# Optimization experiments

Hardware: AMD Instinct MI355X
Metric: run time of the kernel (lower is better)

## Reference

```python
import jax, jax.numpy as jnp
import numpy as np

C = 5.0          # tanh clamp constant (args.c, non-trainable)
B, N, R, D = 4, 16, 64, 256  # batch, block_num, block_len, word_dim
NEG = -1e9


def setup_inputs() -> dict:
    key = jax.random.key(0)
    ks = iter(jax.random.split(key, 80))

    def W(i, o):
        # xavier-like init (torch stores (out,in); we store (in,out) and use x @ W)
        return jax.random.normal(next(ks), (i, o), jnp.float32) * np.float32(np.sqrt(2.0 / (i + o)))

    def bvec(d):
        return jax.random.normal(next(ks), (d,), jnp.float32) * 0.01

    inp = {"x": jax.random.normal(next(ks), (B, N, R, D), jnp.float32)}
    for p in ("fw", "bw"):
        inp[f"fcW_{p}"] = W(D, D);  inp[f"fcb_{p}"] = bvec(D)
        inp[f"mW1_{p}"] = W(D, D);  inp[f"mW2_{p}"] = W(D, D);  inp[f"mb_{p}"] = bvec(D)
        inp[f"s2tW1_{p}"] = W(D, D); inp[f"s2tb1_{p}"] = bvec(D)
        inp[f"s2tW_{p}"] = W(D, D);  inp[f"s2tb_{p}"] = bvec(D)
        inp[f"gW1_{p}"] = W(D, D);  inp[f"gW2_{p}"] = W(D, D);  inp[f"gb_{p}"] = bvec(D)
        inp[f"fW1_{p}"] = W(3 * D, D); inp[f"fb1_{p}"] = bvec(D)
        inp[f"fW2_{p}"] = W(3 * D, D); inp[f"fb2_{p}"] = bvec(D)
    return inp


def _mSA(x, W1, W2, b, fw):
    # x: (..., L, d) -> (..., L, d). Additive per-feature attention with strict
    # triangular mask. fw: token i attends to j > i (last row zeroed);
    # bw: token i attends to j < i (first row zeroed). Matches the torch
    # -inf mask + narrow + zero-pad construction exactly.
    L = x.shape[-2]
    xi = (x @ W1)[..., :, None, :]                 # (..., L, 1, d)
    xj = (x @ W2)[..., None, :, :]                 # (..., 1, L, d)
    f = C * jnp.tanh((xi + xj + b) / C)            # (..., i, j, d)
    i = jnp.arange(L)[:, None]
    j = jnp.arange(L)[None, :]
    allowed = (j > i) if fw else (j < i)           # (L, L)
    scores = jnp.where(allowed[..., None], f, NEG)
    att = jax.nn.softmax(scores, axis=-2)          # softmax over j
    rowvalid = (jnp.arange(L) < L - 1) if fw else (jnp.arange(L) > 0)
    att = att * rowvalid[:, None, None].astype(x.dtype)
    return jnp.einsum('...ijd,...jd->...id', att, x)


def _s2t(x, W1, b1, Wo, bo):
    # source2token self-attention: (..., L, d) -> (..., d)
    f = jax.nn.relu(x @ W1 + b1)
    a = jax.nn.softmax(f @ Wo + bo, axis=-2)
    return jnp.sum(a * x, axis=-2)


def _mblosa(x, mW1, mW2, mb, s2tW1, s2tb1, s2tW, s2tb,
            gW1, gW2, gb, fW1, fb1, fW2, fb2, fw):
    Bb, n, r, d = x.shape
    h = _mSA(x, mW1, mW2, mb, fw)                  # (B, n, r, d) intra-block
    v = _s2t(h, s2tW1, s2tb1, s2tW, s2tb)          # (B, n, d)    block summary
    o = _mSA(v, mW1, mW2, mb, fw)                  # (B, n, d)    inter-block
    G = jax.nn.sigmoid(o @ gW1 + v @ gW2 + gb)
    e = G * o + (1.0 - G) * v                      # (B, n, d)
    # torch: cat of e[i] repeated r times, then narrow(1, 0, n)
    idx = jnp.arange(n) // r
    E = e[:, idx]                                  # (B, n, d)
    # torch: flatten blocks then narrow(1, 0, n) (faithful to source)
    xf = x.reshape(Bb, n * r, d)[:, :n]
    hf = h.reshape(Bb, n * r, d)[:, :n]
    cat = jnp.concatenate([xf, hf, E], axis=-1)    # (B, n, 3d)
    fusion = jax.nn.relu(cat @ fW1 + fb1)
    Gf = jax.nn.sigmoid(cat @ fW2 + fb2)
    return Gf * fusion + (1.0 - Gf) * xf           # (B, n, d)


def reference(x,
              fcW_fw, fcb_fw, mW1_fw, mW2_fw, mb_fw, s2tW1_fw, s2tb1_fw,
              s2tW_fw, s2tb_fw, gW1_fw, gW2_fw, gb_fw, fW1_fw, fb1_fw,
              fW2_fw, fb2_fw,
              fcW_bw, fcb_bw, mW1_bw, mW2_bw, mb_bw, s2tW1_bw, s2tb1_bw,
              s2tW_bw, s2tb_bw, gW1_bw, gW2_bw, gb_bw, fW1_bw, fb1_bw,
              fW2_bw, fb2_bw):
    in_fw = jax.nn.relu(x @ fcW_fw + fcb_fw)
    in_bw = jax.nn.relu(x @ fcW_bw + fcb_bw)
    u_fw = _mblosa(in_fw, mW1_fw, mW2_fw, mb_fw, s2tW1_fw, s2tb1_fw,
                   s2tW_fw, s2tb_fw, gW1_fw, gW2_fw, gb_fw,
                   fW1_fw, fb1_fw, fW2_fw, fb2_fw, True)
    u_bw = _mblosa(in_bw, mW1_bw, mW2_bw, mb_bw, s2tW1_bw, s2tb1_bw,
                   s2tW_bw, s2tb_bw, gW1_bw, gW2_bw, gb_bw,
                   fW1_bw, fb1_bw, fW2_bw, fb2_bw, False)
    return jnp.concatenate([u_fw, u_bw], axis=-1)  # (B, n, 2d)
```

## Files before the change

### kernel.cpp

```cpp
#include <hip/hip_runtime.h>
#include <hip/hip_bf16.h>

typedef __hip_bfloat16 BF16;
typedef __attribute__((ext_vector_type(8))) short short8;
typedef __attribute__((ext_vector_type(4))) float f32x4;

#define MFMA_B16(a,b,c) __builtin_amdgcn_mfma_f32_16x16x32_bf16((a),(b),(c),0,0,0)

#if __has_builtin(__builtin_amdgcn_exp2f)
#define EXP2F(x) __builtin_amdgcn_exp2f(x)
#else
#define EXP2F(x) __expf(0.6931471805599453f * (x))
#endif

__device__ __forceinline__ short f2bs(float f){ BF16 h = __float2bfloat16(f); return *(short*)&h; }
__device__ __forceinline__ float bs2f(short s){ BF16 h = *(BF16*)&s; return __bfloat162float(h); }

struct SrcPack { const float* s[10]; };

__global__ __launch_bounds__(256) void prep_k(SrcPack p, short* __restrict__ Oh,
                                              short* __restrict__ Ol)
{
    __shared__ float s[64][65];
    const float* W = p.s[blockIdx.y];
    short* oh = Oh + (size_t)blockIdx.y * 65536;
    short* ol = Ol + (size_t)blockIdx.y * 65536;
    int tr = (blockIdx.x >> 2) * 64, tc = (blockIdx.x & 3) * 64;
    #pragma unroll
    for (int i = 0; i < 16; i++) {
        int e = threadIdx.x + i * 256;
        int r = e >> 6, c = e & 63;
        s[c][r] = W[(size_t)(tr + r) * 256 + tc + c];
    }
    __syncthreads();
    #pragma unroll
    for (int i = 0; i < 16; i++) {
        int e = threadIdx.x + i * 256;
        int c2 = e >> 6, r2 = e & 63;
        float v = s[c2][r2];
        short hi = f2bs(v);
        short lo = f2bs(v - bs2f(hi));
        size_t oi = (size_t)(tc + c2) * 256 + tr + r2;
        oh[oi] = hi;
        ol[oi] = lo;
    }
}

template<int AM, int OM, int RELU, int BS>
__device__ __forceinline__ void gemm_body(const void* __restrict__ A0,
    const void* __restrict__ Alo,
    const short* __restrict__ Wh, const short* __restrict__ Wl,
    const float* __restrict__ bias, void* __restrict__ O0, void* __restrict__ O1,
    int row0, int col0)
{
    constexpr int LDK = 72;
    __shared__ short sAh[64 * LDK];
    __shared__ short sAl[(AM == 0) ? 8 : 64 * LDK];
    __shared__ short sBh[64 * LDK];
    __shared__ short sBl[BS ? 8 : 64 * LDK];
    int tid = threadIdx.x;
    int w = tid >> 6, l = tid & 63;
    int m = l & 15, q = l >> 4;
    int sr = w * 16 + m;

    f32x4 acc[4];
    #pragma unroll
    for (int cf = 0; cf < 4; cf++) acc[cf] = (f32x4)(0.f);

    for (int kh = 0; kh < 4; kh++) {
        int kbase = kh * 64;
        #pragma unroll
        for (int i = 0; i < 2; i++) {
            int kl = q * 8 + 32 * i;
            size_t gofs = (size_t)(row0 + sr) * 256 + kbase + kl;
            if (AM == 1) {
                const float* src = (const float*)A0 + gofs;
                float4 f0 = *(const float4*)src;
                float4 f1 = *(const float4*)(src + 4);
                short8 vh, vl;
                float tmp[8] = {f0.x, f0.y, f0.z, f0.w, f1.x, f1.y, f1.z, f1.w};
                #pragma unroll
                for (int j = 0; j < 8; j++) {
                    vh[j] = f2bs(tmp[j]);
                    vl[j] = f2bs(tmp[j] - bs2f(vh[j]));
                }
                *(short8*)&sAh[sr * LDK + kl] = vh;
                *(short8*)&sAl[sr * LDK + kl] = vl;
            } else if (AM == 2) {
                *(short8*)&sAh[sr * LDK + kl] = *(const short8*)((const short*)A0 + gofs);
                *(short8*)&sAl[sr * LDK + kl] = *(const short8*)((const short*)Alo + gofs);
            } else {
                *(short8*)&sAh[sr * LDK + kl] = *(const short8*)((const short*)A0 + gofs);
            }
            size_t gofsB = (size_t)(col0 + sr) * 256 + kbase + kl;
            *(short8*)&sBh[sr * LDK + kl] = *(const short8*)(Wh + gofsB);
            if (!BS)
                *(short8*)&sBl[sr * LDK + kl] = *(const short8*)(Wl + gofsB);
        }
        __syncthreads();
        #pragma unroll
        for (int ch = 0; ch < 2; ch++) {
            int k = ch * 32 + q * 8;
            short8 ah = *(const short8*)&sAh[(w * 16 + m) * LDK + k];
            short8 al = (AM != 0) ? *(const short8*)&sAl[(w * 16 + m) * LDK + k] : ah;
            #pragma unroll
            for (int cf = 0; cf < 4; cf++) {
                short8 bh = *(const short8*)&sBh[(cf * 16 + m) * LDK + k];
                acc[cf] = MFMA_B16(ah, bh, acc[cf]);
                if (!BS) {
                    short8 bl = *(const short8*)&sBl[(cf * 16 + m) * LDK + k];
                    acc[cf] = MFMA_B16(ah, bl, acc[cf]);
                }
                if (AM != 0)
                    acc[cf] = MFMA_B16(al, bh, acc[cf]);
            }
        }
        __syncthreads();
    }
    #pragma unroll
    for (int cf = 0; cf < 4; cf++) {
        int col = col0 + cf * 16 + m;
        float bv = bias ? bias[col] : 0.f;
        #pragma unroll
        for (int r = 0; r < 4; r++) {
            int row = row0 + w * 16 + q * 4 + r;
            float v = acc[cf][r] + bv;
            if (RELU) v = fmaxf(v, 0.f);
            size_t oi = (size_t)row * 256 + col;
            if (OM == 0) {
                ((float*)O0)[oi] = v;
            } else if (OM == 1) {
                ((short*)O0)[oi] = f2bs(v);
            } else {
                short hi = f2bs(v);
                ((short*)O0)[oi] = hi;
                ((short*)O1)[oi] = f2bs(v - bs2f(hi));
            }
        }
    }
}

struct GDir { const void* A0; const void* Al; const short* Wh; const short* Wl;
              const float* bias; void* O0; void* O1; };

template<int AM, int OM, int RELU, int BS>
__global__ __launch_bounds__(256) void gemm_k(GDir p0, GDir p1)
{
    GDir p = blockIdx.z ? p1 : p0;
    gemm_body<AM, OM, RELU, BS>(p.A0, p.Al, p.Wh, p.Wl, p.bias, p.O0, p.O1,
                                blockIdx.x * 64, blockIdx.y * 64);
}

struct MbloDir { const short* Ah;
                 const short* W1h; const short* W2h;
                 const float* mb; short* Hh; int fw; };

__global__ __launch_bounds__(512) void mblo_k(MbloDir p0, MbloDir p1)
{
    __shared__ char smraw[33536] __attribute__((aligned(16)));
    short* gAh  = (short*)smraw;
    short* gB1h = gAh + 4608;
    short* gB2h = gAh + 9216;
    float* aP   = (float*)smraw;
    unsigned int* aQX = (unsigned int*)(smraw + 16896);

    const float KLN = -0.06931471805599453f;

    MbloDir p = blockIdx.z ? p1 : p0;
    int tid = threadIdx.x;
    int w = tid >> 6, l = tid & 63;
    int m = l & 15, q = l >> 4;
    int rh = w >> 1;
    int cb = (w & 1) * 2;
    int bn = blockIdx.x >> 1, ipar = blockIdx.x & 1;
    int row0 = bn * 64, d0 = blockIdx.y * 64;
    int srow = tid >> 3;
    int skl  = (tid & 7) * 8;

    f32x4 acc1[2], acc2[2];
    #pragma unroll
    for (int cf = 0; cf < 2; cf++) { acc1[cf] = (f32x4)(0.f); acc2[cf] = (f32x4)(0.f); }

    for (int kh = 0; kh < 4; kh++) {
        int kbase = kh * 64;
        size_t ga = (size_t)(row0 + srow) * 256 + kbase + skl;
        *(short8*)&gAh[srow * 72 + skl] = *(const short8*)(p.Ah + ga);
        size_t gb = (size_t)(d0 + srow) * 256 + kbase + skl;
        *(short8*)&gB1h[srow * 72 + skl] = *(const short8*)(p.W1h + gb);
        *(short8*)&gB2h[srow * 72 + skl] = *(const short8*)(p.W2h + gb);
        __syncthreads();
        #pragma unroll
        for (int ch = 0; ch < 2; ch++) {
            int k = ch * 32 + q * 8;
            short8 ah = *(const short8*)&gAh[(rh * 16 + m) * 72 + k];
            #pragma unroll
            for (int cf = 0; cf < 2; cf++) {
                int bofs = ((cb + cf) * 16 + m) * 72 + k;
                short8 b1 = *(const short8*)&gB1h[bofs];
                acc1[cf] = MFMA_B16(ah, b1, acc1[cf]);
                short8 b2 = *(const short8*)&gB2h[bofs];
                acc2[cf] = MFMA_B16(ah, b2, acc2[cf]);
            }
        }
        __syncthreads();
    }
    short* sQX = (short*)aQX;
    #pragma unroll
    for (int cf = 0; cf < 2; cf++) {
        int col = (cb + cf) * 16 + m;
        float mbv = p.mb[d0 + col];
        #pragma unroll
        for (int r = 0; r < 4; r++) {
            int row = rh * 16 + q * 4 + r;
            aP[row * 66 + col] = __expf(0.4f * acc1[cf][r]) * KLN;
            sQX[col * 130 + 2 * row] = f2bs(__expf(0.4f * (acc2[cf][r] + mbv)));
        }
    }
    {
        size_t gx = (size_t)(row0 + srow) * 256 + d0 + skl;
        short8 xh = *(const short8*)(p.Ah + gx);
        #pragma unroll
        for (int t = 0; t < 8; t++)
            sQX[(skl + t) * 130 + 2 * srow + 1] = xh[t];
    }
    __syncthreads();
    const unsigned int* lane_qx = &aQX[l * 65];
    #pragma unroll
    for (int t8 = 0; t8 < 4; t8++) {
        int i = ipar + 2 * (w + 8 * t8);
        float Pp = aP[i * 66 + l];
        int js = p.fw ? (i + 1) : 0;
        int je = p.fw ? 64 : i;
        float den0 = 0.f, den1 = 0.f, num0 = 0.f, num1 = 0.f;
        int j = js;
        for (; j + 4 <= je; j += 4) {
            unsigned int u0 = lane_qx[j];
            unsigned int u1 = lane_qx[j + 1];
            unsigned int u2 = lane_qx[j + 2];
            unsigned int u3 = lane_qx[j + 3];
            float q0 = bs2f((short)(u0 & 0xffff)), x0 = bs2f((short)(u0 >> 16));
            float q1 = bs2f((short)(u1 & 0xffff)), x1 = bs2f((short)(u1 >> 16));
            float q2 = bs2f((short)(u2 & 0xffff)), x2 = bs2f((short)(u2 >> 16));
            float q3 = bs2f((short)(u3 & 0xffff)), x3 = bs2f((short)(u3 >> 16));
            float w0 = EXP2F(__builtin_amdgcn_rcpf(fmaf(Pp, q0, KLN)));
            float w1 = EXP2F(__builtin_amdgcn_rcpf(fmaf(Pp, q1, KLN)));
            float w2 = EXP2F(__builtin_amdgcn_rcpf(fmaf(Pp, q2, KLN)));
            float w3 = EXP2F(__builtin_amdgcn_rcpf(fmaf(Pp, q3, KLN)));
            den0 += w0; num0 = fmaf(w0, x0, num0);
            den1 += w1; num1 = fmaf(w1, x1, num1);
            den0 += w2; num0 = fmaf(w2, x2, num0);
            den1 += w3; num1 = fmaf(w3, x3, num1);
        }
        for (; j < je; j++) {
            unsigned int u0 = lane_qx[j];
            float q0 = bs2f((short)(u0 & 0xffff)), x0 = bs2f((short)(u0 >> 16));
            float wgt = EXP2F(__builtin_amdgcn_rcpf(fmaf(Pp, q0, KLN)));
            den0 += wgt; num0 = fmaf(wgt, x0, num0);
        }
        float den = den0 + den1, num = num0 + num1;
        bool valid = p.fw ? (i < 63) : (i > 0);
        float out = valid ? (num * __builtin_amdgcn_rcpf(den)) : 0.f;
        p.Hh[(size_t)(row0 + i) * 256 + d0 + l] = f2bs(out);
    }
}

struct S2TDir { const short* Hh; const short* W3h; const float* b1;
                const short* W4h; const float* b2; float* V; };

__global__ __launch_bounds__(512) void s2t_fused_k(S2TDir p0, S2TDir p1)
{
    __shared__ char smraw[79872] __attribute__((aligned(16)));
    short* sT1 = (short*)smraw;
    short* gA  = (short*)(smraw + 33792);
    short* gB  = (short*)(smraw + 43008);
    short* gB2 = (short*)(smraw + 33792);
    float* aL  = (float*)(smraw + 43008);
    float* rm  = (float*)(smraw + 60416);
    float* rd  = rm + 512;
    float* rn  = rm + 1024;

    S2TDir p = blockIdx.z ? p1 : p0;
    int tid = threadIdx.x;
    int w = tid >> 6, l = tid & 63;
    int m = l & 15, q = l >> 4;
    int row0 = blockIdx.x * 64;
    int strip = w >> 1, chalf = w & 1;
    int srow = tid >> 3, skl = (tid & 7) * 8;

    f32x4 acc1[8];
    #pragma unroll
    for (int cf = 0; cf < 8; cf++) acc1[cf] = (f32x4)(0.f);
    for (int kh = 0; kh < 4; kh++) {
        int kbase = kh * 64;
        *(short8*)&gA[srow * 72 + skl] =
            *(const short8*)(p.Hh + (size_t)(row0 + srow) * 256 + kbase + skl);
        int bn = tid >> 1;
        #pragma unroll
        for (int i = 0; i < 4; i++) {
            int kseg = (tid & 1) * 32 + i * 8;
            *(short8*)&gB[bn * 72 + kseg] =
                *(const short8*)(p.W3h + (size_t)bn * 256 + kbase + kseg);
        }
        __syncthreads();
        #pragma unroll
        for (int ch = 0; ch < 2; ch++) {
            int k = ch * 32 + q * 8;
            short8 ah = *(const short8*)&gA[(strip * 16 + m) * 72 + k];
            #pragma unroll
            for (int cf = 0; cf < 8; cf++) {
                short8 bh = *(const short8*)&gB[(chalf * 128 + cf * 16 + m) * 72 + k];
                acc1[cf] = MFMA_B16(ah, bh, acc1[cf]);
            }
        }
        __syncthreads();
    }
    #pragma unroll
    for (int cf = 0; cf < 8; cf++) {
        int col = chalf * 128 + cf * 16 + m;
        float bv = p.b1[col];
        #pragma unroll
        for (int r = 0; r < 4; r++) {
            int row = strip * 16 + q * 4 + r;
            sT1[row * 264 + col] = f2bs(fmaxf(acc1[cf][r] + bv, 0.f));
        }
    }
    __syncthreads();

    for (int dc = 0; dc < 2; dc++) {
        int d0 = (blockIdx.y * 2 + dc) * 64;
        f32x4 acc2[2];
        acc2[0] = (f32x4)(0.f); acc2[1] = (f32x4)(0.f);
        for (int kh = 0; kh < 4; kh++) {
            int kbase = kh * 64;
            *(short8*)&gB2[srow * 72 + skl] =
                *(const short8*)(p.W4h + (size_t)(d0 + srow) * 256 + kbase + skl);
            __syncthreads();
            #pragma unroll
            for (int ch = 0; ch < 2; ch++) {
                int k = ch * 32 + q * 8;
                short8 ah = *(const short8*)&sT1[(strip * 16 + m) * 264 + kbase + k];
                #pragma unroll
                for (int cf = 0; cf < 2; cf++) {
                    short8 bh = *(const short8*)&gB2[(chalf * 32 + cf * 16 + m) * 72 + k];
                    acc2[cf] = MFMA_B16(ah, bh, acc2[cf]);
                }
            }
            __syncthreads();
        }
        #pragma unroll
        for (int cf = 0; cf < 2; cf++) {
            int col = chalf * 32 + cf * 16 + m;
            float bv = p.b2[d0 + col];
            #pragma unroll
            for (int r = 0; r < 4; r++) {
                int row = strip * 16 + q * 4 + r;
                aL[row * 68 + col] = acc2[cf][r] + bv;
            }
        }
        __syncthreads();
        int dl = tid & 63, rq = tid >> 6;
        float mx = -1e30f, den = 0.f, num = 0.f;
        #pragma unroll
        for (int rr = 0; rr < 8; rr++) {
            int r = rq * 8 + rr;
            float lv = aL[r * 68 + dl];
            float hv = bs2f(p.Hh[(size_t)(row0 + r) * 256 + d0 + dl]);
            if (lv > mx) { float sc = __expf(mx - lv); den *= sc; num *= sc; mx = lv; }
            float wgt = __expf(lv - mx);
            den += wgt; num = fmaf(wgt, hv, num);
        }
        rm[rq * 64 + dl] = mx; rd[rq * 64 + dl] = den; rn[rq * 64 + dl] = num;
        __syncthreads();
        if (rq == 0) {
            float M = rm[dl];
            #pragma unroll
            for (int kq = 1; kq < 8; kq++) M = fmaxf(M, rm[kq * 64 + dl]);
            float D = 0.f, Nn = 0.f;
            #pragma unroll
            for (int kq = 0; kq < 8; kq++) {
                float sc = __expf(rm[kq * 64 + dl] - M);
                D += rd[kq * 64 + dl] * sc;
                Nn += rn[kq * 64 + dl] * sc;
            }
            p.V[(size_t)blockIdx.x * 256 + d0 + dl] = Nn / D;
        }
        __syncthreads();
    }
}

struct Gate2Dir { const float* V; const float* W1; const float* W2; const float* mb;
                  const float* gW1; const float* gW2; const float* gb;
                  float* E0; int fw; };

__global__ __launch_bounds__(512) void attn2gate_k(Gate2Dir p0, Gate2Dir p1)
{
    Gate2Dir p = blockIdx.z ? p1 : p0;
    __shared__ __attribute__((aligned(16))) float sVT[4096];
    __shared__ float sPart[16][256];
    __shared__ float so[256], sv[256], red[8][64];
    int tid = threadIdx.x;
    int b = blockIdx.x;
    int k = tid & 255, half = tid >> 8;

    if (p.fw) {
        #pragma unroll
        for (int it = 0; it < 8; it++) {
            int e = tid + it * 512;
            int kk = e >> 4, j = e & 15;
            sVT[e] = p.V[(size_t)(b * 16 + j) * 256 + kk];
        }
        __syncthreads();
        float acc[16];
        #pragma unroll
        for (int j = 0; j < 16; j++) acc[j] = 0.f;
        int kk0 = half * 128;
        #pragma unroll 4
        for (int kk = kk0; kk < kk0 + 128; kk++) {
            const float4* vr = (const float4*)&sVT[kk * 16];
            float4 va = vr[0], vb = vr[1], vc = vr[2], vd = vr[3];
            float w1 = p.W1[(size_t)kk * 256 + k];
            float w2 = p.W2[(size_t)kk * 256 + k];
            acc[0]  = fmaf(va.x, w1, acc[0]);
            acc[1]  = fmaf(va.y, w2, acc[1]);
            acc[2]  = fmaf(va.z, w2, acc[2]);
            acc[3]  = fmaf(va.w, w2, acc[3]);
            acc[4]  = fmaf(vb.x, w2, acc[4]);
            acc[5]  = fmaf(vb.y, w2, acc[5]);
            acc[6]  = fmaf(vb.z, w2, acc[6]);
            acc[7]  = fmaf(vb.w, w2, acc[7]);
            acc[8]  = fmaf(vc.x, w2, acc[8]);
            acc[9]  = fmaf(vc.y, w2, acc[9]);
            acc[10] = fmaf(vc.z, w2, acc[10]);
            acc[11] = fmaf(vc.w, w2, acc[11]);
            acc[12] = fmaf(vd.x, w2, acc[12]);
            acc[13] = fmaf(vd.y, w2, acc[13]);
            acc[14] = fmaf(vd.z, w2, acc[14]);
            acc[15] = fmaf(vd.w, w2, acc[15]);
        }
        if (half) {
            #pragma unroll
            for (int j = 0; j < 16; j++) sPart[j][k] = acc[j];
        }
        __syncthreads();
        if (!half) {
            #pragma unroll
            for (int j = 0; j < 16; j++) acc[j] += sPart[j][k];
            float base = acc[0] + p.mb[k];
            float den = 0.f, num = 0.f;
            #pragma unroll
            for (int j = 1; j < 16; j++) {
                float z = (base + acc[j]) * 0.2f;
                float e2 = __expf(2.f * z);
                float t = 1.f - 2.f / (e2 + 1.f);
                float wgt = __expf(5.f * t);
                den += wgt;
                num = fmaf(wgt, p.V[(size_t)(b * 16 + j) * 256 + k], num);
            }
            so[k] = num / den;
            sv[k] = p.V[(size_t)(b * 16) * 256 + k];
        }
    } else {
        if (!half) {
            so[k] = 0.f;
            sv[k] = p.V[(size_t)(b * 16) * 256 + k];
        }
    }
    __syncthreads();
    int c = tid & 63, ks = tid >> 6;
    int gc = blockIdx.y * 64 + c;
    float a2 = 0.f;
    int k0 = ks * 32;
    #pragma unroll 8
    for (int kkx = 0; kkx < 32; kkx++) {
        int kx = k0 + kkx;
        a2 += so[kx] * p.gW1[(size_t)kx * 256 + gc] + sv[kx] * p.gW2[(size_t)kx * 256 + gc];
    }
    red[ks][c] = a2;
    __syncthreads();
    if (ks == 0) {
        float a = red[0][c] + red[1][c] + red[2][c] + red[3][c]
                + red[4][c] + red[5][c] + red[6][c] + red[7][c] + p.gb[gc];
        float G = 1.f / (1.f + __expf(-a));
        p.E0[b * 256 + gc] = G * so[gc] + (1.f - G) * sv[gc];
    }
}

struct FuseDir { const short* INh; const short* Hh;
                 const float* E0; const float* fW1; const float* fb1;
                 const float* fW2; const float* fb2; };

__global__ __launch_bounds__(256) void fusion_k(FuseDir p0, FuseDir p1, float* __restrict__ out)
{
    FuseDir p = blockIdx.z ? p1 : p0;
    __shared__ float cat[768];
    __shared__ float red1[4][64], red2[4][64];
    int bt = blockIdx.x, b = bt >> 4, t = bt & 15;
    int c = threadIdx.x & 63, ks = threadIdx.x >> 6;
    int gc = blockIdx.y * 64 + c;
    size_t xrow = ((size_t)b * 1024 + t) * 256;
    cat[threadIdx.x]       = bs2f(p.INh[xrow + threadIdx.x]);
    cat[256 + threadIdx.x] = bs2f(p.Hh[xrow + threadIdx.x]);
    cat[512 + threadIdx.x] = p.E0[b * 256 + threadIdx.x];
    __syncthreads();
    float a1 = 0.f, a2 = 0.f;
    int k0 = ks * 192;
    #pragma unroll 8
    for (int kk = 0; kk < 192; kk++) {
        int k = k0 + kk;
        float cv = cat[k];
        a1 += cv * p.fW1[(size_t)k * 256 + gc];
        a2 += cv * p.fW2[(size_t)k * 256 + gc];
    }
    red1[ks][c] = a1; red2[ks][c] = a2;
    __syncthreads();
    if (ks == 0) {
        float s1 = red1[0][c] + red1[1][c] + red1[2][c] + red1[3][c] + p.fb1[gc];
        float s2 = red2[0][c] + red2[1][c] + red2[2][c] + red2[3][c] + p.fb2[gc];
        float fus = fmaxf(s1, 0.f);
        float Gf = 1.f / (1.f + __expf(-s2));
        float u = Gf * fus + (1.f - Gf) * cat[gc];
        out[((size_t)(b * 16 + t)) * 512 + (size_t)blockIdx.z * 256 + gc] = u;
    }
}

extern "C" void kernel_launch(void* const* d_in, const int* in_sizes, int n_in,
                              void* d_out, int out_size, void* d_ws, size_t ws_size,
                              hipStream_t stream)
{
    const float* x = (const float*)d_in[0];
    char* base = (char*)d_ws;
    auto alloc = [&](size_t bytes){ void* r = base; base += (bytes + 255) & ~255ULL; return r; };
    short* inH = (short*)alloc(2 * 1048576 * 2);
    short* hH  = (short*)alloc(2 * 1048576 * 2);
    short* wtH = (short*)alloc(10 * 65536 * 2);
    short* wtL = (short*)alloc(10 * 65536 * 2);
    float* v   = (float*)alloc(2 * 16384 * 4);
    float* E0  = (float*)alloc(2 * 1024 * 4);

    SrcPack sp;
    const int src_idx[5] = {0, 2, 3, 5, 7};
    for (int p = 0; p < 2; p++)
        for (int i = 0; i < 5; i++)
            sp.s[p * 5 + i] = (const float*)d_in[1 + p * 16 + src_idx[i]];
    prep_k<<<dim3(16, 10), 256, 0, stream>>>(sp, wtH, wtL);

    GDir fc[2];
    MbloDir mbd[2];
    S2TDir std[2];
    Gate2Dir gtd[2];
    FuseDir fsd[2];
    for (int p = 0; p < 2; p++) {
        int bi = 1 + p * 16;
        const float* fcb   = (const float*)d_in[bi + 1];
        const float* mb    = (const float*)d_in[bi + 4];
        const float* s2tb1 = (const float*)d_in[bi + 6];
        const float* s2tb  = (const float*)d_in[bi + 8];
        size_t po = (size_t)p * 1048576;
        const short* W0h = wtH + (size_t)(p * 5 + 0) * 65536, *W0l = wtL + (size_t)(p * 5 + 0) * 65536;
        const short* W1h = wtH + (size_t)(p * 5 + 1) * 65536;
        const short* W2h = wtH + (size_t)(p * 5 + 2) * 65536;
        const short* W3h = wtH + (size_t)(p * 5 + 3) * 65536;
        const short* W4h = wtH + (size_t)(p * 5 + 4) * 65536;

        fc[p]   = { x, nullptr, W0h, W0l, fcb, inH + po, nullptr };
        mbd[p]  = { inH + po, W1h, W2h, mb, hH + po, (p == 0) };
        std[p]  = { hH + po, W3h, s2tb1, W4h, s2tb, v + p * 16384 };
        gtd[p]  = { v + p * 16384,
                    (const float*)d_in[bi + 2], (const float*)d_in[bi + 3], mb,
                    (const float*)d_in[bi + 9], (const float*)d_in[bi + 10],
                    (const float*)d_in[bi + 11], E0 + p * 1024, (p == 0) };
        fsd[p]  = { inH + po, hH + po, E0 + p * 1024,
                    (const float*)d_in[bi + 12], (const float*)d_in[bi + 13],
                    (const float*)d_in[bi + 14], (const float*)d_in[bi + 15] };
    }

    gemm_k<1, 1, 1, 0><<<dim3(64, 4, 2), 256, 0, stream>>>(fc[0], fc[1]);
    mblo_k<<<dim3(128, 4, 2), 512, 0, stream>>>(mbd[0], mbd[1]);
    s2t_fused_k<<<dim3(64, 2, 2), 512, 0, stream>>>(std[0], std[1]);
    attn2gate_k<<<dim3(4, 4, 2), 512, 0, stream>>>(gtd[0], gtd[1]);
    fusion_k<<<dim3(64, 4, 2), 256, 0, stream>>>(fsd[0], fsd[1], (float*)d_out);
}
```

Baseline: 207.8 us.

## Fuse weight prep into fc GEMM kernel and widen s2t grid

Merges the weight transpose/bf16-split prep kernel with the input fc GEMM into one launch. The fc GEMM blocks now read fp32 W0 directly and split it into hi/lo bf16 in-kernel, while extra blocks convert the other weights to bf16-hi only; the unused lo buffer is dropped. This removes one launch and a serial dependency between prep and fc. The s2t kernel now handles one 64-column chunk per block with a doubled grid instead of looping over two chunks, which adds parallelism but recomputes the first-stage GEMM per block. The strided uncoalesced W0 column reads in the fc path may cost bandwidth.

Measured after the change: 207.3 us. Within noise of the previous version (-0.3%).

```diff
diff --git a/kernel.cpp b/kernel.cpp
--- a/kernel.cpp
+++ b/kernel.cpp
@@ -16,52 +16,58 @@
 __device__ __forceinline__ short f2bs(float f){ BF16 h = __float2bfloat16(f); return *(short*)&h; }
 __device__ __forceinline__ float bs2f(short s){ BF16 h = *(BF16*)&s; return __bfloat162float(h); }
 
-struct SrcPack { const float* s[10]; };
-
-__global__ __launch_bounds__(256) void prep_k(SrcPack p, short* __restrict__ Oh,
-                                              short* __restrict__ Ol)
+struct FcPrepP {
+    const float* X;
+    const float* W0[2];
+    const float* fcb[2];
+    short* inH[2];
+    const float* wsrc[8];
+    short* wdst[8];
+};
+
+__global__ __launch_bounds__(256) void fcprep_k(FcPrepP P)
 {
-    __shared__ float s[64][65];
-    const float* W = p.s[blockIdx.y];
-    short* oh = Oh + (size_t)blockIdx.y * 65536;
-    short* ol = Ol + (size_t)blockIdx.y * 65536;
-    int tr = (blockIdx.x >> 2) * 64, tc = (blockIdx.x & 3) * 64;
-    #pragma unroll
-    for (int i = 0; i < 16; i++) {
-        int e = threadIdx.x + i * 256;
-        int r = e >> 6, c = e & 63;
-        s[c][r] = W[(size_t)(tr + r) * 256 + tc + c];
-    }
-    __syncthreads();
-    #pragma unroll
-    for (int i = 0; i < 16; i++) {
-        int e = threadIdx.x + i * 256;
-        int c2 = e >> 6, r2 = e & 63;
-        float v = s[c2][r2];
-        short hi = f2bs(v);
-        short lo = f2bs(v - bs2f(hi));
-        size_t oi = (size_t)(tc + c2) * 256 + tr + r2;
-        oh[oi] = hi;
-        ol[oi] = lo;
-    }
-}
-
-template<int AM, int OM, int RELU, int BS>
-__device__ __forceinline__ void gemm_body(const void* __restrict__ A0,
-    const void* __restrict__ Alo,
-    const short* __restrict__ Wh, const short* __restrict__ Wl,
-    const float* __restrict__ bias, void* __restrict__ O0, void* __restrict__ O1,
-    int row0, int col0)
-{
-    constexpr int LDK = 72;
-    __shared__ short sAh[64 * LDK];
-    __shared__ short sAl[(AM == 0) ? 8 : 64 * LDK];
-    __shared__ short sBh[64 * LDK];
-    __shared__ short sBl[BS ? 8 : 64 * LDK];
+    __shared__ char SM[36864] __attribute__((aligned(16)));
+    int job = blockIdx.x;
     int tid = threadIdx.x;
+
+    if (job >= 512) {
+        int mi = job - 512;
+        int mat = mi >> 4, tile = mi & 15;
+        float (*s)[65] = (float(*)[65])SM;
+        const float* W = P.wsrc[mat];
+        short* oh = P.wdst[mat];
+        int tr = (tile >> 2) * 64, tc = (tile & 3) * 64;
+        #pragma unroll
+        for (int i = 0; i < 16; i++) {
+            int e = tid + i * 256;
+            int r = e >> 6, c = e & 63;
+            s[c][r] = W[(size_t)(tr + r) * 256 + tc + c];
+        }
+        __syncthreads();
+        #pragma unroll
+        for (int i = 0; i < 16; i++) {
+            int e = tid + i * 256;
+            int c2 = e >> 6, r2 = e & 63;
+            oh[(size_t)(tc + c2) * 256 + tr + r2] = f2bs(s[c2][r2]);
+        }
+        return;
+    }
+
+    short* sAh = (short*)SM;
+    short* sAl = sAh + 4608;
+    short* sBh = sAh + 9216;
+    short* sBl = sAh + 13824;
+    int dir = job >> 8, rem = job & 255;
+    int row0 = (rem & 63) * 64, col0 = (rem >> 6) * 64;
+    const float* W0 = P.W0[dir];
+    const float* bias = P.fcb[dir];
+    short* O = P.inH[dir];
+
     int w = tid >> 6, l = tid & 63;
     int m = l & 15, q = l >> 4;
     int sr = w * 16 + m;
+    int bcc = tid >> 2, bkk0 = (tid & 3) * 16;
 
     f32x4 acc[4];
     #pragma unroll
@@ -73,46 +79,50 @@
         for (int i = 0; i < 2; i++) {
             int kl = q * 8 + 32 * i;
             size_t gofs = (size_t)(row0 + sr) * 256 + kbase + kl;
-            if (AM == 1) {
-                const float* src = (const float*)A0 + gofs;
-                float4 f0 = *(const float4*)src;
-                float4 f1 = *(const float4*)(src + 4);
+            const float* src = P.X + gofs;
+            float4 f0 = *(const float4*)src;
+            float4 f1 = *(const float4*)(src + 4);
+            short8 vh, vl;
+            float tmp[8] = {f0.x, f0.y, f0.z, f0.w, f1.x, f1.y, f1.z, f1.w};
+            #pragma unroll
+            for (int j = 0; j < 8; j++) {
+                vh[j] = f2bs(tmp[j]);
+                vl[j] = f2bs(tmp[j] - bs2f(vh[j]));
+            }
+            *(short8*)&sAh[sr * 72 + kl] = vh;
+            *(short8*)&sAl[sr * 72 + kl] = vl;
+        }
+        {
+            float vals[16];
+            #pragma unroll
+            for (int j = 0; j < 16; j++)
+                vals[j] = W0[(size_t)(kbase + bkk0 + j) * 256 + col0 + bcc];
+            #pragma unroll
+            for (int h8 = 0; h8 < 2; h8++) {
                 short8 vh, vl;
-                float tmp[8] = {f0.x, f0.y, f0.z, f0.w, f1.x, f1.y, f1.z, f1.w};
                 #pragma unroll
                 for (int j = 0; j < 8; j++) {
-                    vh[j] = f2bs(tmp[j]);
-                    vl[j] = f2bs(tmp[j] - bs2f(vh[j]));
+                    float v = vals[h8 * 8 + j];
+                    vh[j] = f2bs(v);
+                    vl[j] = f2bs(v - bs2f(vh[j]));
                 }
-                *(short8*)&sAh[sr * LDK + kl] = vh;
-                *(short8*)&sAl[sr * LDK + kl] = vl;
-            } else if (AM == 2) {
-                *(short8*)&sAh[sr * LDK + kl] = *(const short8*)((const short*)A0 + gofs);
-                *(short8*)&sAl[sr * LDK + kl] = *(const short8*)((const short*)Alo + gofs);
-            } else {
-                *(short8*)&sAh[sr * LDK + kl] = *(const short8*)((const short*)A0 + gofs);
-            }
-            size_t gofsB = (size_t)(col0 + sr) * 256 + kbase + kl;
-            *(short8*)&sBh[sr * LDK + kl] = *(const short8*)(Wh + gofsB);
-            if (!BS)
-                *(short8*)&sBl[sr * LDK + kl] = *(const short8*)(Wl + gofsB);
+                *(short8*)&sBh[bcc * 72 + bkk0 + h8 * 8] = vh;
+                *(short8*)&sBl[bcc * 72 + bkk0 + h8 * 8] = vl;
+            }
         }
         __syncthreads();
         #pragma unroll
         for (int ch = 0; ch < 2; ch++) {
             int k = ch * 32 + q * 8;
-            short8 ah = *(const short8*)&sAh[(w * 16 + m) * LDK + k];
-            short8 al = (AM != 0) ? *(const short8*)&sAl[(w * 16 + m) * LDK + k] : ah;
+            short8 ah = *(const short8*)&sAh[(w * 16 + m) * 72 + k];
+            short8 al = *(const short8*)&sAl[(w * 16 + m) * 72 + k];
             #pragma unroll
             for (int cf = 0; cf < 4; cf++) {
-                short8 bh = *(const short8*)&sBh[(cf * 16 + m) * LDK + k];
+                short8 bh = *(const short8*)&sBh[(cf * 16 + m) * 72 + k];
                 acc[cf] = MFMA_B16(ah, bh, acc[cf]);
-                if (!BS) {
-                    short8 bl = *(const short8*)&sBl[(cf * 16 + m) * LDK + k];
-                    acc[cf] = MFMA_B16(ah, bl, acc[cf]);
-                }
-                if (AM != 0)
-                    acc[cf] = MFMA_B16(al, bh, acc[cf]);
+                short8 bl = *(const short8*)&sBl[(cf * 16 + m) * 72 + k];
+                acc[cf] = MFMA_B16(ah, bl, acc[cf]);
+                acc[cf] = MFMA_B16(al, bh, acc[cf]);
             }
         }
         __syncthreads();
@@ -120,39 +130,17 @@
     #pragma unroll
     for (int cf = 0; cf < 4; cf++) {
         int col = col0 + cf * 16 + m;
-        float bv = bias ? bias[col] : 0.f;
+        float bv = bias[col];
         #pragma unroll
         for (int r = 0; r < 4; r++) {
             int row = row0 + w * 16 + q * 4 + r;
-            float v = acc[cf][r] + bv;
-            if (RELU) v = fmaxf(v, 0.f);
-            size_t oi = (size_t)row * 256 + col;
-            if (OM == 0) {
-                ((float*)O0)[oi] = v;
-            } else if (OM == 1) {
-                ((short*)O0)[oi] = f2bs(v);
-            } else {
-                short hi = f2bs(v);
-                ((short*)O0)[oi] = hi;
-                ((short*)O1)[oi] = f2bs(v - bs2f(hi));
-            }
+            float v = fmaxf(acc[cf][r] + bv, 0.f);
+            O[(size_t)row * 256 + col] = f2bs(v);
         }
     }
 }
 
-struct GDir { const void* A0; const void* Al; const short* Wh; const short* Wl;
-              const float* bias; void* O0; void* O1; };
-
-template<int AM, int OM, int RELU, int BS>
-__global__ __launch_bounds__(256) void gemm_k(GDir p0, GDir p1)
-{
-    GDir p = blockIdx.z ? p1 : p0;
-    gemm_body<AM, OM, RELU, BS>(p.A0, p.Al, p.Wh, p.Wl, p.bias, p.O0, p.O1,
-                                blockIdx.x * 64, blockIdx.y * 64);
-}
-
-struct MbloDir { const short* Ah;
-                 const short* W1h; const short* W2h;
+struct MbloDir { const short* Ah; const short* W1h; const short* W2h;
                  const float* mb; short* Hh; int fw; };
 
 __global__ __launch_bounds__(512) void mblo_k(MbloDir p0, MbloDir p1)
@@ -284,6 +272,7 @@
     int w = tid >> 6, l = tid & 63;
     int m = l & 15, q = l >> 4;
     int row0 = blockIdx.x * 64;
+    int d0 = blockIdx.y * 64;
     int strip = w >> 1, chalf = w & 1;
     int srow = tid >> 3, skl = (tid & 7) * 8;
 
@@ -326,65 +315,61 @@
     }
     __syncthreads();
 
-    for (int dc = 0; dc < 2; dc++) {
-        int d0 = (blockIdx.y * 2 + dc) * 64;
-        f32x4 acc2[2];
-        acc2[0] = (f32x4)(0.f); acc2[1] = (f32x4)(0.f);
-        for (int kh = 0; kh < 4; kh++) {
-            int kbase = kh * 64;
-            *(short8*)&gB2[srow * 72 + skl] =
-                *(const short8*)(p.W4h + (size_t)(d0 + srow) * 256 + kbase + skl);
-            __syncthreads();
-            #pragma unroll
-            for (int ch = 0; ch < 2; ch++) {
-                int k = ch * 32 + q * 8;
-                short8 ah = *(const short8*)&sT1[(strip * 16 + m) * 264 + kbase + k];
-                #pragma unroll
-                for (int cf = 0; cf < 2; cf++) {
-                    short8 bh = *(const short8*)&gB2[(chalf * 32 + cf * 16 + m) * 72 + k];
-                    acc2[cf] = MFMA_B16(ah, bh, acc2[cf]);
-                }
-            }
-            __syncthreads();
-        }
-        #pragma unroll
-        for (int cf = 0; cf < 2; cf++) {
-            int col = chalf * 32 + cf * 16 + m;
-            float bv = p.b2[d0 + col];
-            #pragma unroll
-            for (int r = 0; r < 4; r++) {
-                int row = strip * 16 + q * 4 + r;
-                aL[row * 68 + col] = acc2[cf][r] + bv;
-            }
-        }
-        __syncthreads();
-        int dl = tid & 63, rq = tid >> 6;
-        float mx = -1e30f, den = 0.f, num = 0.f;
-        #pragma unroll
-        for (int rr = 0; rr < 8; rr++) {
-            int r = rq * 8 + rr;
-            float lv = aL[r * 68 + dl];
-            float hv = bs2f(p.Hh[(size_t)(row0 + r) * 256 + d0 + dl]);
-            if (lv > mx) { float sc = __expf(mx - lv); den *= sc; num *= sc; mx = lv; }
-            float wgt = __expf(lv - mx);
-            den += wgt; num = fmaf(wgt, hv, num);
-        }
-        rm[rq * 64 + dl] = mx; rd[rq * 64 + dl] = den; rn[rq * 64 + dl] = num;
-        __syncthreads();
-        if (rq == 0) {
-            float M = rm[dl];
-            #pragma unroll
-            for (int kq = 1; kq < 8; kq++) M = fmaxf(M, rm[kq * 64 + dl]);
-            float D = 0.f, Nn = 0.f;
-            #pragma unroll
-            for (int kq = 0; kq < 8; kq++) {
-                float sc = __expf(rm[kq * 64 + dl] - M);
-                D += rd[kq * 64 + dl] * sc;
-                Nn += rn[kq * 64 + dl] * sc;
-            }
-            p.V[(size_t)blockIdx.x * 256 + d0 + dl] = Nn / D;
-        }
-        __syncthreads();
+    f32x4 acc2[2];
+    acc2[0] = (f32x4)(0.f); acc2[1] = (f32x4)(0.f);
+    for (int kh = 0; kh < 4; kh++) {
+        int kbase = kh * 64;
+        *(short8*)&gB2[srow * 72 + skl] =
+            *(const short8*)(p.W4h + (size_t)(d0 + srow) * 256 + kbase + skl);
+        __syncthreads();
+        #pragma unroll
+        for (int ch = 0; ch < 2; ch++) {
+            int k = ch * 32 + q * 8;
+            short8 ah = *(const short8*)&sT1[(strip * 16 + m) * 264 + kbase + k];
+            #pragma unroll
+            for (int cf = 0; cf < 2; cf++) {
+                short8 bh = *(const short8*)&gB2[(chalf * 32 + cf * 16 + m) * 72 + k];
+                acc2[cf] = MFMA_B16(ah, bh, acc2[cf]);
+            }
+        }
+        __syncthreads();
+    }
+    #pragma unroll
+    for (int cf = 0; cf < 2; cf++) {
+        int col = chalf * 32 + cf * 16 + m;
+        float bv = p.b2[d0 + col];
+        #pragma unroll
+        for (int r = 0; r < 4; r++) {
+            int row = strip * 16 + q * 4 + r;
+            aL[row * 68 + col] = acc2[cf][r] + bv;
+        }
+    }
+    __syncthreads();
+    int dl = tid & 63, rq = tid >> 6;
+    float mx = -1e30f, den = 0.f, num = 0.f;
+    #pragma unroll
+    for (int rr = 0; rr < 8; rr++) {
+        int r = rq * 8 + rr;
+        float lv = aL[r * 68 + dl];
+        float hv = bs2f(p.Hh[(size_t)(row0 + r) * 256 + d0 + dl]);
+        if (lv > mx) { float sc = __expf(mx - lv); den *= sc; num *= sc; mx = lv; }
+        float wgt = __expf(lv - mx);
+        den += wgt; num = fmaf(wgt, hv, num);
+    }
+    rm[rq * 64 + dl] = mx; rd[rq * 64 + dl] = den; rn[rq * 64 + dl] = num;
+    __syncthreads();
+    if (rq == 0) {
+        float M = rm[dl];
+        #pragma unroll
+        for (int kq = 1; kq < 8; kq++) M = fmaxf(M, rm[kq * 64 + dl]);
+        float D = 0.f, Nn = 0.f;
+        #pragma unroll
+        for (int kq = 0; kq < 8; kq++) {
+            float sc = __expf(rm[kq * 64 + dl] - M);
+            D += rd[kq * 64 + dl] * sc;
+            Nn += rn[kq * 64 + dl] * sc;
+        }
+        p.V[(size_t)blockIdx.x * 256 + d0 + dl] = Nn / D;
     }
 }
 
@@ -533,38 +518,40 @@
     short* inH = (short*)alloc(2 * 1048576 * 2);
     short* hH  = (short*)alloc(2 * 1048576 * 2);
     short* wtH = (short*)alloc(10 * 65536 * 2);
-    short* wtL = (short*)alloc(10 * 65536 * 2);
     float* v   = (float*)alloc(2 * 16384 * 4);
     float* E0  = (float*)alloc(2 * 1024 * 4);
 
-    SrcPack sp;
-    const int src_idx[5] = {0, 2, 3, 5, 7};
-    for (int p = 0; p < 2; p++)
-        for (int i = 0; i < 5; i++)
-            sp.s[p * 5 + i] = (const float*)d_in[1 + p * 16 + src_idx[i]];
-    prep_k<<<dim3(16, 10), 256, 0, stream>>>(sp, wtH, wtL);
-
-    GDir fc[2];
+    FcPrepP fp;
+    fp.X = x;
+    const int wsrc_idx[4] = {2, 3, 5, 7};
+    for (int p = 0; p < 2; p++) {
+        int bi = 1 + p * 16;
+        fp.W0[p]  = (const float*)d_in[bi + 0];
+        fp.fcb[p] = (const float*)d_in[bi + 1];
+        fp.inH[p] = inH + (size_t)p * 1048576;
+        for (int wi = 0; wi < 4; wi++) {
+            fp.wsrc[p * 4 + wi] = (const float*)d_in[bi + wsrc_idx[wi]];
+            fp.wdst[p * 4 + wi] = wtH + (size_t)(p * 5 + 1 + wi) * 65536;
+        }
+    }
+
     MbloDir mbd[2];
-    S2TDir std[2];
+    S2TDir std_[2];
     Gate2Dir gtd[2];
     FuseDir fsd[2];
     for (int p = 0; p < 2; p++) {
         int bi = 1 + p * 16;
-        const float* fcb   = (const float*)d_in[bi + 1];
         const float* mb    = (const float*)d_in[bi + 4];
         const float* s2tb1 = (const float*)d_in[bi + 6];
         const float* s2tb  = (const float*)d_in[bi + 8];
         size_t po = (size_t)p * 1048576;
-        const short* W0h = wtH + (size_t)(p * 5 + 0) * 65536, *W0l = wtL + (size_t)(p * 5 + 0) * 65536;
         const short* W1h = wtH + (size_t)(p * 5 + 1) * 65536;
         const short* W2h = wtH + (size_t)(p * 5 + 2) * 65536;
         const short* W3h = wtH + (size_t)(p * 5 + 3) * 65536;
         const short* W4h = wtH + (size_t)(p * 5 + 4) * 65536;
 
-        fc[p]   = { x, nullptr, W0h, W0l, fcb, inH + po, nullptr };
         mbd[p]  = { inH + po, W1h, W2h, mb, hH + po, (p == 0) };
-        std[p]  = { hH + po, W3h, s2tb1, W4h, s2tb, v + p * 16384 };
+        std_[p] = { hH + po, W3h, s2tb1, W4h, s2tb, v + p * 16384 };
         gtd[p]  = { v + p * 16384,
                     (const float*)d_in[bi + 2], (const float*)d_in[bi + 3], mb,
                     (const float*)d_in[bi + 9], (const float*)d_in[bi + 10],
@@ -574,9 +561,9 @@
                     (const float*)d_in[bi + 14], (const float*)d_in[bi + 15] };
     }
 
-    gemm_k<1, 1, 1, 0><<<dim3(64, 4, 2), 256, 0, stream>>>(fc[0], fc[1]);
+    fcprep_k<<<dim3(640), 256, 0, stream>>>(fp);
     mblo_k<<<dim3(128, 4, 2), 512, 0, stream>>>(mbd[0], mbd[1]);
-    s2t_fused_k<<<dim3(64, 2, 2), 512, 0, stream>>>(std[0], std[1]);
+    s2t_fused_k<<<dim3(64, 4, 2), 512, 0, stream>>>(std_[0], std_[1]);
     attn2gate_k<<<dim3(4, 4, 2), 512, 0, stream>>>(gtd[0], gtd[1]);
     fusion_k<<<dim3(64, 4, 2), 256, 0, stream>>>(fsd[0], fsd[1], (float*)d_out);
 }
```
